# Optimization experiments

Measured on AMD Instinct MI355X. Metric: run time of the kernel, lower is better.

The kernel has to match this reference:

```python
import jax, jax.numpy as jnp
import numpy as np

N = 100_000      # nodes
D = 64           # in_dim
E = 1_600_000    # edges (avg degree 16)
P_L = 0.5        # leaky slope for low-pass gate
P_H = 0.5        # leaky slope for high-pass gate


def setup_inputs() -> dict:
    key = jax.random.key(0)
    ks = jax.random.split(key, 10)
    h = jax.random.normal(ks[0], (N, D), jnp.float32)
    d = jax.random.uniform(ks[1], (N,), jnp.float32)  # degree norms 1/sqrt(deg)
    src = jax.random.randint(ks[2], (E,), 0, N)
    dst = jax.random.randint(ks[3], (E,), 0, N)
    # xavier_normal(gain=1.414) scale ~ gain*sqrt(2/(fan_in+fan_out))
    sg = 1.414 * np.sqrt(2.0 / (2 * D + 1))
    sr = 1.414 * np.sqrt(2.0 / (2 * D + D))
    Wl = jax.random.normal(ks[4], (1, 2 * D), jnp.float32) * sg
    bl = jnp.zeros((1,), jnp.float32)
    Wh = jax.random.normal(ks[5], (1, 2 * D), jnp.float32) * sg
    bh = jnp.zeros((1,), jnp.float32)
    Wr = jax.random.normal(ks[6], (D, 2 * D), jnp.float32) * sr
    br = jnp.zeros((D,), jnp.float32)
    return {"h": h, "d": d, "src": src, "dst": dst,
            "Wl": Wl, "bl": bl, "Wh": Wh, "bh": bh, "Wr": Wr, "br": br}


def reference(h, d, src, dst, Wl, bl, Wh, bh, Wr, br):
    # gate_x(cat([h_dst, h_src])) == h_dst @ W[:, :D] + h_src @ W[:, D:] + b
    # -> project once per node [N], gather per edge [E] (avoids [E,2D] concat)
    low_dst = h @ Wl[0, :D]
    low_src = h @ Wl[0, D:]
    _low = low_dst[dst] + low_src[src] + bl[0]                     # [E]
    g_low = jnp.tanh(jax.nn.relu(jnp.where(_low > 0, _low, -P_L * _low)))

    high_dst = h @ Wh[0, :D]
    high_src = h @ Wh[0, D:]
    _high = high_dst[dst] + high_src[src] + bh[0]                  # [E]
    g_high = jnp.tanh(-jax.nn.relu(jnp.where(_high > 0, _high, -P_H * _high)))

    dd = d[dst] * d[src]                                           # [E]
    e_low = g_low * dd
    e_high = g_high * dd

    h_src = h[src]                                                 # [E, D]
    z_low = jax.ops.segment_sum(h_src * e_low[:, None], dst, num_segments=N)
    z_high = jax.ops.segment_sum(h_src * e_high[:, None], dst, num_segments=N)

    z = jnp.concatenate([z_low, z_high], axis=1)                   # [N, 2D]
    return z @ Wr.T + br                                           # [N, D]
```

## Files before the change

### kernel.cpp

```cpp
#include <hip/hip_runtime.h>
#include <hip/hip_fp16.h>
#include <math.h>

#define N_NODES 100000
#define D_DIM   64
#define N_EDGES 1600000
#define P_L 0.5f
#define P_H 0.5f

#define NPB   32
#define NB    3125
#define TILE  8192
#define NT    ((N_EDGES + TILE - 1) / TILE)
#define CAP   768
#define ZS    132

typedef unsigned int uint;
typedef unsigned short ushort_t;

__device__ inline ushort_t f2bf(float f) {
    uint u = __float_as_uint(f);
    uint r = (u + 0x7fffu + ((u >> 16) & 1u)) >> 16;
    return (ushort_t)r;
}

__device__ inline float tanh_pos(float x) {
    return 1.f - 2.f / (__expf(2.f * x) + 1.f);
}

__global__ __launch_bounds__(256) void node_gates_kernel(
    const float* __restrict__ h, const float* __restrict__ dvec,
    const float* __restrict__ Wl, const float* __restrict__ Wh,
    ushort_t* __restrict__ hbf,
    float4* __restrict__ gdst4, float4* __restrict__ gsrc4)
{
    int tid = threadIdx.x;
    int node = blockIdx.x * 4 + (tid >> 6);
    if (node >= N_NODES) return;
    int lane = tid & 63;

    float hv = h[(size_t)node * 64 + lane];
    hbf[(size_t)node * 64 + lane] = f2bf(hv);

    float pld = hv * Wl[lane];
    float pls = hv * Wl[64 + lane];
    float phd = hv * Wh[lane];
    float phs = hv * Wh[64 + lane];
    #pragma unroll
    for (int m = 32; m >= 1; m >>= 1) {
        pld += __shfl_xor(pld, m);
        pls += __shfl_xor(pls, m);
        phd += __shfl_xor(phd, m);
        phs += __shfl_xor(phs, m);
    }
    if (lane == 0) {
        float d = dvec[node];
        gdst4[node] = make_float4(pld, phd, d, 0.f);
        gsrc4[node] = make_float4(pls, phs, d, 0.f);
    }
}

__global__ __launch_bounds__(1024) void bucket_hist_kernel(const int* __restrict__ dst,
                                                           int* __restrict__ T) {
    __shared__ int hist[NB];
    int tid = threadIdx.x;
    for (int i = tid; i < NB; i += 1024) hist[i] = 0;
    __syncthreads();
    int base = blockIdx.x * TILE;
    #pragma unroll
    for (int j = 0; j < TILE / 1024; ++j) {
        int e = base + j * 1024 + tid;
        if (e < N_EDGES) atomicAdd(&hist[dst[e] >> 5], 1);
    }
    __syncthreads();
    int* row = T + (size_t)blockIdx.x * NB;
    for (int i = tid; i < NB; i += 1024) row[i] = hist[i];
}

__global__ __launch_bounds__(1024) void scanA_kernel(int* __restrict__ T,
                                                     int* __restrict__ totG) {
    int b = blockIdx.x * 1024 + threadIdx.x;
    if (b >= NB) return;
    int run = 0;
    for (int w = 0; w < NT; ++w) {
        int idx = w * NB + b;
        int v = T[idx];
        T[idx] = run;
        run += v;
    }
    totG[b] = run;
}

__global__ __launch_bounds__(1024) void scanB_kernel(const int* __restrict__ totG,
                                                     int* __restrict__ baseG,
                                                     int* __restrict__ bucketoffs,
                                                     const float* __restrict__ Wr,
                                                     float* __restrict__ wrt) {
    int tid = threadIdx.x;
    for (int idx = tid; idx < 64 * 128; idx += 1024) {
        int c = idx >> 7;
        int k = idx & 127;
        wrt[k * 64 + c] = Wr[idx];
    }

    __shared__ int scan_lds[1024];
    int a[4];
    int s = 0;
    #pragma unroll
    for (int i = 0; i < 4; ++i) {
        int b = tid * 4 + i;
        a[i] = (b < NB) ? totG[b] : 0;
        s += a[i];
    }
    scan_lds[tid] = s;
    __syncthreads();
    for (int d = 1; d < 1024; d <<= 1) {
        int v = (tid >= d) ? scan_lds[tid - d] : 0;
        __syncthreads();
        scan_lds[tid] += v;
        __syncthreads();
    }
    int excl = scan_lds[tid] - s;
    int total = scan_lds[1023];
    #pragma unroll
    for (int i = 0; i < 4; ++i) {
        int b = tid * 4 + i;
        if (b < NB) { baseG[b] = excl; bucketoffs[b] = excl; }
        excl += a[i];
    }
    if (tid == 0) bucketoffs[NB] = total;
}

__global__ __launch_bounds__(1024) void place_kernel(
    const int* __restrict__ src, const int* __restrict__ dst,
    const int* __restrict__ T, const int* __restrict__ baseG,
    const float4* __restrict__ gdst4, const float4* __restrict__ gsrc4,
    const float* __restrict__ bl, const float* __restrict__ bh,
    uint2* __restrict__ ebuf)
{
    __shared__ int cur[NB];
    int tid = threadIdx.x;
    const int* row = T + (size_t)blockIdx.x * NB;
    for (int i = tid; i < NB; i += 1024) cur[i] = row[i] + baseG[i];
    __syncthreads();

    float bl0 = bl[0], bh0 = bh[0];
    int base = blockIdx.x * TILE;
    #pragma unroll
    for (int j = 0; j < TILE / 1024; ++j) {
        int e = base + j * 1024 + tid;
        if (e >= N_EDGES) continue;
        int t = dst[e];
        int s = src[e];
        float4 gt = gdst4[t];
        float4 gs = gsrc4[s];
        float xl = gt.x + gs.x + bl0;
        float xh = gt.y + gs.y + bh0;
        float ll = xl > 0.f ? xl : -P_L * xl;
        float hh = xh > 0.f ? xh : -P_H * xh;
        float dd = gt.z * gs.z;
        float el =  tanh_pos(ll) * dd;
        float eh = -tanh_pos(hh) * dd;
        uint ge = (uint)__half_as_ushort(__float2half_rn(el))
                | ((uint)__half_as_ushort(__float2half_rn(eh)) << 16);
        int b  = t >> 5;
        uint dl = (uint)(t & 31);
        int pos = atomicAdd(&cur[b], 1);
        ebuf[pos] = make_uint2((uint)s | (dl << 17), ge);
    }
}

__global__ __launch_bounds__(512) void accum_final_kernel(
    const int* __restrict__ bucketoffs, const uint2* __restrict__ ebuf,
    const ushort_t* __restrict__ hbf, const float* __restrict__ wrt,
    const float* __restrict__ br, float* __restrict__ out)
{
    __shared__ float z[NPB * ZS];
    __shared__ uint2 srec[CAP];
    __shared__ int ncount[NPB];
    __shared__ int nbase[NPB];
    __shared__ int ncur[NPB];

    int tid = threadIdx.x;
    int bk = blockIdx.x;
    int beg = bucketoffs[bk];
    int end = bucketoffs[bk + 1];
    int cnt = end - beg;
    if (cnt > CAP) cnt = CAP;

    if (tid < NPB) ncount[tid] = 0;

    bool hA = tid < cnt;
    bool hB = tid + 512 < cnt;
    uint2 rA = hA ? ebuf[beg + tid] : make_uint2(0, 0);
    uint2 rB = hB ? ebuf[beg + tid + 512] : make_uint2(0, 0);
    __syncthreads();

    if (hA) atomicAdd(&ncount[(rA.x >> 17) & 31], 1);
    if (hB) atomicAdd(&ncount[(rB.x >> 17) & 31], 1);
    __syncthreads();

    if (tid < 32) {
        int v = ncount[tid];
        int p = v;
        #pragma unroll
        for (int d = 1; d < 32; d <<= 1) {
            int x = __shfl_up(p, d);
            if (tid >= d) p += x;
        }
        nbase[tid] = p - v;
        ncur[tid]  = p - v;
    }
    __syncthreads();

    if (hA) {
        int dl = (rA.x >> 17) & 31;
        srec[atomicAdd(&ncur[dl], 1)] = rA;
    }
    if (hB) {
        int dl = (rB.x >> 17) & 31;
        srec[atomicAdd(&ncur[dl], 1)] = rB;
    }
    __syncthreads();

    int sg = tid >> 3;
    int l8 = tid & 7;
    int node4 = sg >> 1;
    int par = sg & 1;
    int rbeg = nbase[node4];
    int rend = ncur[node4];

    float acc[16];
    #pragma unroll
    for (int j = 0; j < 16; ++j) acc[j] = 0.f;

    int k = rbeg + par;
    for (; k + 6 < rend; k += 8) {
        uint2 r0 = srec[k];
        uint2 r1 = srec[k + 2];
        uint2 r2 = srec[k + 4];
        uint2 r3 = srec[k + 6];
        uint4 h0 = *(const uint4*)(hbf + (size_t)(r0.x & 0x1FFFF) * 64 + l8 * 8);
        uint4 h1 = *(const uint4*)(hbf + (size_t)(r1.x & 0x1FFFF) * 64 + l8 * 8);
        uint4 h2 = *(const uint4*)(hbf + (size_t)(r2.x & 0x1FFFF) * 64 + l8 * 8);
        uint4 h3 = *(const uint4*)(hbf + (size_t)(r3.x & 0x1FFFF) * 64 + l8 * 8);

        #pragma unroll
        for (int u = 0; u < 4; ++u) {
            uint gy = (u == 0) ? r0.y : (u == 1) ? r1.y : (u == 2) ? r2.y : r3.y;
            uint4 hv = (u == 0) ? h0 : (u == 1) ? h1 : (u == 2) ? h2 : h3;
            float el = __half2float(__ushort_as_half((unsigned short)(gy & 0xffffu)));
            float eh = __half2float(__ushort_as_half((unsigned short)(gy >> 16)));
            float f0 = __uint_as_float(hv.x << 16);
            float f1 = __uint_as_float(hv.x & 0xffff0000u);
            float f2 = __uint_as_float(hv.y << 16);
            float f3 = __uint_as_float(hv.y & 0xffff0000u);
            float f4 = __uint_as_float(hv.z << 16);
            float f5 = __uint_as_float(hv.z & 0xffff0000u);
            float f6 = __uint_as_float(hv.w << 16);
            float f7 = __uint_as_float(hv.w & 0xffff0000u);
            acc[0]  += el * f0; acc[1]  += el * f1; acc[2]  += el * f2; acc[3]  += el * f3;
            acc[4]  += el * f4; acc[5]  += el * f5; acc[6]  += el * f6; acc[7]  += el * f7;
            acc[8]  += eh * f0; acc[9]  += eh * f1; acc[10] += eh * f2; acc[11] += eh * f3;
            acc[12] += eh * f4; acc[13] += eh * f5; acc[14] += eh * f6; acc[15] += eh * f7;
        }
    }
    for (; k < rend; k += 2) {
        uint2 r0 = srec[k];
        uint4 hv = *(const uint4*)(hbf + (size_t)(r0.x & 0x1FFFF) * 64 + l8 * 8);
        float el = __half2float(__ushort_as_half((unsigned short)(r0.y & 0xffffu)));
        float eh = __half2float(__ushort_as_half((unsigned short)(r0.y >> 16)));
        float f0 = __uint_as_float(hv.x << 16);
        float f1 = __uint_as_float(hv.x & 0xffff0000u);
        float f2 = __uint_as_float(hv.y << 16);
        float f3 = __uint_as_float(hv.y & 0xffff0000u);
        float f4 = __uint_as_float(hv.z << 16);
        float f5 = __uint_as_float(hv.z & 0xffff0000u);
        float f6 = __uint_as_float(hv.w << 16);
        float f7 = __uint_as_float(hv.w & 0xffff0000u);
        acc[0]  += el * f0; acc[1]  += el * f1; acc[2]  += el * f2; acc[3]  += el * f3;
        acc[4]  += el * f4; acc[5]  += el * f5; acc[6]  += el * f6; acc[7]  += el * f7;
        acc[8]  += eh * f0; acc[9]  += eh * f1; acc[10] += eh * f2; acc[11] += eh * f3;
        acc[12] += eh * f4; acc[13] += eh * f5; acc[14] += eh * f6; acc[15] += eh * f7;
    }

    float* zp = &z[node4 * ZS + l8 * 8];
    if (par == 0) {
        *(float4*)(zp + 0)  = make_float4(acc[0],  acc[1],  acc[2],  acc[3]);
        *(float4*)(zp + 4)  = make_float4(acc[4],  acc[5],  acc[6],  acc[7]);
        *(float4*)(zp + 64) = make_float4(acc[8],  acc[9],  acc[10], acc[11]);
        *(float4*)(zp + 68) = make_float4(acc[12], acc[13], acc[14], acc[15]);
    }
    __syncthreads();
    if (par == 1) {
        float4 z0 = *(float4*)(zp + 0);
        float4 z1 = *(float4*)(zp + 4);
        float4 z2 = *(float4*)(zp + 64);
        float4 z3 = *(float4*)(zp + 68);
        *(float4*)(zp + 0)  = make_float4(z0.x + acc[0],  z0.y + acc[1],  z0.z + acc[2],  z0.w + acc[3]);
        *(float4*)(zp + 4)  = make_float4(z1.x + acc[4],  z1.y + acc[5],  z1.z + acc[6],  z1.w + acc[7]);
        *(float4*)(zp + 64) = make_float4(z2.x + acc[8],  z2.y + acc[9],  z2.z + acc[10], z2.w + acc[11]);
        *(float4*)(zp + 68) = make_float4(z3.x + acc[12], z3.y + acc[13], z3.z + acc[14], z3.w + acc[15]);
    }
    __syncthreads();

    int node = tid >> 4;
    int g = tid & 15;
    float facc[4] = {0.f, 0.f, 0.f, 0.f};
    const float* zrow = z + node * ZS;
    #pragma unroll 4
    for (int kk = 0; kk < 128; ++kk) {
        float zv = zrow[kk];
        float4 w = *(const float4*)(wrt + kk * 64 + g * 4);
        facc[0] += zv * w.x; facc[1] += zv * w.y; facc[2] += zv * w.z; facc[3] += zv * w.w;
    }
    int n = bk * NPB + node;
    float* op = out + (size_t)n * 64 + g * 4;
    const float* bp = br + g * 4;
    *(float4*)(op) = make_float4(facc[0] + bp[0], facc[1] + bp[1], facc[2] + bp[2], facc[3] + bp[3]);
}

extern "C" void kernel_launch(void* const* d_in, const int* in_sizes, int n_in,
                              void* d_out, int out_size, void* d_ws, size_t ws_size,
                              hipStream_t stream) {
    const float* h    = (const float*)d_in[0];
    const float* dvec = (const float*)d_in[1];
    const int*   src  = (const int*)  d_in[2];
    const int*   dst  = (const int*)  d_in[3];
    const float* Wl   = (const float*)d_in[4];
    const float* bl   = (const float*)d_in[5];
    const float* Wh   = (const float*)d_in[6];
    const float* bh   = (const float*)d_in[7];
    const float* Wr   = (const float*)d_in[8];
    const float* br   = (const float*)d_in[9];
    float* out = (float*)d_out;

    char* ws = (char*)d_ws;
    size_t off = 0;
    auto alloc = [&](size_t bytes) { char* p = ws + off; off += (bytes + 255) & ~size_t(255); return p; };

    ushort_t* hbf       = (ushort_t*)alloc((size_t)N_NODES * 64 * 2);
    float4*   gdst4     = (float4*)  alloc((size_t)N_NODES * 16);
    float4*   gsrc4     = (float4*)  alloc((size_t)N_NODES * 16);
    float*    wrt       = (float*)   alloc(64 * 128 * 4);
    int*      T         = (int*)     alloc((size_t)NT * NB * 4);
    int*      totG      = (int*)     alloc((size_t)NB * 4);
    int*      baseG     = (int*)     alloc((size_t)NB * 4);
    int*      bucketoffs= (int*)     alloc((size_t)(NB + 1) * 4);
    uint2*    ebuf      = (uint2*)   alloc((size_t)N_EDGES * 8);

    node_gates_kernel<<<(N_NODES + 3) / 4, 256, 0, stream>>>(h, dvec, Wl, Wh, hbf, gdst4, gsrc4);
    bucket_hist_kernel<<<NT, 1024, 0, stream>>>(dst, T);
    scanA_kernel<<<(NB + 1023) / 1024, 1024, 0, stream>>>(T, totG);
    scanB_kernel<<<1, 1024, 0, stream>>>(totG, baseG, bucketoffs, Wr, wrt);
    place_kernel<<<NT, 1024, 0, stream>>>(src, dst, T, baseG, gdst4, gsrc4, bl, bh, ebuf);
    accum_final_kernel<<<NB, 512, 0, stream>>>(bucketoffs, ebuf, hbf, wrt, br, out);
}
```

Before: 317.2 us.

## Split column scan into two-level grouped scan and deepen gather unroll

The serial per-bucket scan over all 196 histogram tiles becomes a two-level scan: 28 groups of 7 tiles are scanned in parallel, then a second pass scans the group totals. The place kernel adds the group offset back when it initializes its cursors. In the accumulate kernel, the gather loop now issues 8 independent row loads per step instead of 4, and a launch-bounds occupancy hint is added. This targets the latency of the nearly serial scan (only 4 blocks, 196 dependent iterations) and raises memory-level parallelism in the gather, at the cost of one extra kernel launch and possibly more register pressure.

```diff
diff --git a/kernel.cpp b/kernel.cpp
--- a/kernel.cpp
+++ b/kernel.cpp
@@ -12,8 +12,11 @@
 #define NB    3125
 #define TILE  8192
 #define NT    ((N_EDGES + TILE - 1) / TILE)
+#define GRP   28
+#define GT    7
 #define CAP   768
 #define ZS    132
+
 
 typedef unsigned int uint;
 typedef unsigned short ushort_t;
@@ -26,6 +29,23 @@
 
 __device__ inline float tanh_pos(float x) {
     return 1.f - 2.f / (__expf(2.f * x) + 1.f);
+}
+
+__device__ inline void fma16(uint gy, uint4 hv, float* acc) {
+    float el = __half2float(__ushort_as_half((unsigned short)(gy & 0xffffu)));
+    float eh = __half2float(__ushort_as_half((unsigned short)(gy >> 16)));
+    float f0 = __uint_as_float(hv.x << 16);
+    float f1 = __uint_as_float(hv.x & 0xffff0000u);
+    float f2 = __uint_as_float(hv.y << 16);
+    float f3 = __uint_as_float(hv.y & 0xffff0000u);
+    float f4 = __uint_as_float(hv.z << 16);
+    float f5 = __uint_as_float(hv.z & 0xffff0000u);
+    float f6 = __uint_as_float(hv.w << 16);
+    float f7 = __uint_as_float(hv.w & 0xffff0000u);
+    acc[0]  += el * f0; acc[1]  += el * f1; acc[2]  += el * f2; acc[3]  += el * f3;
+    acc[4]  += el * f4; acc[5]  += el * f5; acc[6]  += el * f6; acc[7]  += el * f7;
+    acc[8]  += eh * f0; acc[9]  += eh * f1; acc[10] += eh * f2; acc[11] += eh * f3;
+    acc[12] += eh * f4; acc[13] += eh * f5; acc[14] += eh * f6; acc[15] += eh * f7;
 }
 
 __global__ __launch_bounds__(256) void node_gates_kernel(
@@ -77,15 +97,32 @@
     for (int i = tid; i < NB; i += 1024) row[i] = hist[i];
 }
 
-__global__ __launch_bounds__(1024) void scanA_kernel(int* __restrict__ T,
-                                                     int* __restrict__ totG) {
+__global__ __launch_bounds__(1024) void scanA1_kernel(int* __restrict__ T,
+                                                      int* __restrict__ S) {
+    int b = blockIdx.x * 1024 + threadIdx.x;
+    if (b >= NB) return;
+    int g = blockIdx.y;
+    int run = 0;
+    #pragma unroll
+    for (int w = g * GT; w < g * GT + GT; ++w) {
+        int idx = w * NB + b;
+        int v = T[idx];
+        T[idx] = run;
+        run += v;
+    }
+    S[(size_t)g * NB + b] = run;
+}
+
+__global__ __launch_bounds__(1024) void scanA2_kernel(int* __restrict__ S,
+                                                      int* __restrict__ totG) {
     int b = blockIdx.x * 1024 + threadIdx.x;
     if (b >= NB) return;
     int run = 0;
-    for (int w = 0; w < NT; ++w) {
-        int idx = w * NB + b;
-        int v = T[idx];
-        T[idx] = run;
+    #pragma unroll
+    for (int g = 0; g < GRP; ++g) {
+        int idx = g * NB + b;
+        int v = S[idx];
+        S[idx] = run;
         run += v;
     }
     totG[b] = run;
@@ -133,15 +170,17 @@
 
 __global__ __launch_bounds__(1024) void place_kernel(
     const int* __restrict__ src, const int* __restrict__ dst,
-    const int* __restrict__ T, const int* __restrict__ baseG,
+    const int* __restrict__ T, const int* __restrict__ S,
+    const int* __restrict__ baseG,
     const float4* __restrict__ gdst4, const float4* __restrict__ gsrc4,
     const float* __restrict__ bl, const float* __restrict__ bh,
     uint2* __restrict__ ebuf)
 {
     __shared__ int cur[NB];
     int tid = threadIdx.x;
-    const int* row = T + (size_t)blockIdx.x * NB;
-    for (int i = tid; i < NB; i += 1024) cur[i] = row[i] + baseG[i];
+    const int* row  = T + (size_t)blockIdx.x * NB;
+    const int* Srow = S + (size_t)(blockIdx.x / GT) * NB;
+    for (int i = tid; i < NB; i += 1024) cur[i] = row[i] + Srow[i] + baseG[i];
     __syncthreads();
 
     float bl0 = bl[0], bh0 = bh[0];
@@ -170,7 +209,7 @@
     }
 }
 
-__global__ __launch_bounds__(512) void accum_final_kernel(
+__global__ __launch_bounds__(512, 8) void accum_final_kernel(
     const int* __restrict__ bucketoffs, const uint2* __restrict__ ebuf,
     const ushort_t* __restrict__ hbf, const float* __restrict__ wrt,
     const float* __restrict__ br, float* __restrict__ out)
@@ -235,53 +274,34 @@
     for (int j = 0; j < 16; ++j) acc[j] = 0.f;
 
     int k = rbeg + par;
-    for (; k + 6 < rend; k += 8) {
-        uint2 r0 = srec[k];
-        uint2 r1 = srec[k + 2];
-        uint2 r2 = srec[k + 4];
-        uint2 r3 = srec[k + 6];
-        uint4 h0 = *(const uint4*)(hbf + (size_t)(r0.x & 0x1FFFF) * 64 + l8 * 8);
-        uint4 h1 = *(const uint4*)(hbf + (size_t)(r1.x & 0x1FFFF) * 64 + l8 * 8);
-        uint4 h2 = *(const uint4*)(hbf + (size_t)(r2.x & 0x1FFFF) * 64 + l8 * 8);
-        uint4 h3 = *(const uint4*)(hbf + (size_t)(r3.x & 0x1FFFF) * 64 + l8 * 8);
-
-        #pragma unroll
-        for (int u = 0; u < 4; ++u) {
-            uint gy = (u == 0) ? r0.y : (u == 1) ? r1.y : (u == 2) ? r2.y : r3.y;
-            uint4 hv = (u == 0) ? h0 : (u == 1) ? h1 : (u == 2) ? h2 : h3;
-            float el = __half2float(__ushort_as_half((unsigned short)(gy & 0xffffu)));
-            float eh = __half2float(__ushort_as_half((unsigned short)(gy >> 16)));
-            float f0 = __uint_as_float(hv.x << 16);
-            float f1 = __uint_as_float(hv.x & 0xffff0000u);
-            float f2 = __uint_as_float(hv.y << 16);
-            float f3 = __uint_as_float(hv.y & 0xffff0000u);
-            float f4 = __uint_as_float(hv.z << 16);
-            float f5 = __uint_as_float(hv.z & 0xffff0000u);
-            float f6 = __uint_as_float(hv.w << 16);
-            float f7 = __uint_as_float(hv.w & 0xffff0000u);
-            acc[0]  += el * f0; acc[1]  += el * f1; acc[2]  += el * f2; acc[3]  += el * f3;
-            acc[4]  += el * f4; acc[5]  += el * f5; acc[6]  += el * f6; acc[7]  += el * f7;
-            acc[8]  += eh * f0; acc[9]  += eh * f1; acc[10] += eh * f2; acc[11] += eh * f3;
-            acc[12] += eh * f4; acc[13] += eh * f5; acc[14] += eh * f6; acc[15] += eh * f7;
+    while (k + 14 < rend) {
+        uint gy[8]; uint4 hh[8];
+        #pragma unroll
+        for (int i = 0; i < 8; ++i) {
+            uint2 r = srec[k + 2 * i];
+            gy[i] = r.y;
+            hh[i] = *(const uint4*)(hbf + (size_t)(r.x & 0x1FFFF) * 64 + l8 * 8);
         }
+        #pragma unroll
+        for (int i = 0; i < 8; ++i) fma16(gy[i], hh[i], acc);
+        k += 16;
+    }
+    while (k + 6 < rend) {
+        uint gy[4]; uint4 hh[4];
+        #pragma unroll
+        for (int i = 0; i < 4; ++i) {
+            uint2 r = srec[k + 2 * i];
+            gy[i] = r.y;
+            hh[i] = *(const uint4*)(hbf + (size_t)(r.x & 0x1FFFF) * 64 + l8 * 8);
+        }
+        #pragma unroll
+        for (int i = 0; i < 4; ++i) fma16(gy[i], hh[i], acc);
+        k += 8;
     }
     for (; k < rend; k += 2) {
         uint2 r0 = srec[k];
         uint4 hv = *(const uint4*)(hbf + (size_t)(r0.x & 0x1FFFF) * 64 + l8 * 8);
-        float el = __half2float(__ushort_as_half((unsigned short)(r0.y & 0xffffu)));
-        float eh = __half2float(__ushort_as_half((unsigned short)(r0.y >> 16)));
-        float f0 = __uint_as_float(hv.x << 16);
-        float f1 = __uint_as_float(hv.x & 0xffff0000u);
-        float f2 = __uint_as_float(hv.y << 16);
-        float f3 = __uint_as_float(hv.y & 0xffff0000u);
-        float f4 = __uint_as_float(hv.z << 16);
-        float f5 = __uint_as_float(hv.z & 0xffff0000u);
-        float f6 = __uint_as_float(hv.w << 16);
-        float f7 = __uint_as_float(hv.w & 0xffff0000u);
-        acc[0]  += el * f0; acc[1]  += el * f1; acc[2]  += el * f2; acc[3]  += el * f3;
-        acc[4]  += el * f4; acc[5]  += el * f5; acc[6]  += el * f6; acc[7]  += el * f7;
-        acc[8]  += eh * f0; acc[9]  += eh * f1; acc[10] += eh * f2; acc[11] += eh * f3;
-        acc[12] += eh * f4; acc[13] += eh * f5; acc[14] += eh * f6; acc[15] += eh * f7;
+        fma16(r0.y, hv, acc);
     }
 
     float* zp = &z[node4 * ZS + l8 * 8];
@@ -344,6 +364,7 @@
     float4*   gsrc4     = (float4*)  alloc((size_t)N_NODES * 16);
     float*    wrt       = (float*)   alloc(64 * 128 * 4);
     int*      T         = (int*)     alloc((size_t)NT * NB * 4);
+    int*      S         = (int*)     alloc((size_t)GRP * NB * 4);
     int*      totG      = (int*)     alloc((size_t)NB * 4);
     int*      baseG     = (int*)     alloc((size_t)NB * 4);
     int*      bucketoffs= (int*)     alloc((size_t)(NB + 1) * 4);
@@ -351,8 +372,12 @@
 
     node_gates_kernel<<<(N_NODES + 3) / 4, 256, 0, stream>>>(h, dvec, Wl, Wh, hbf, gdst4, gsrc4);
     bucket_hist_kernel<<<NT, 1024, 0, stream>>>(dst, T);
-    scanA_kernel<<<(NB + 1023) / 1024, 1024, 0, stream>>>(T, totG);
+    {
+        dim3 g1((NB + 1023) / 1024, GRP);
+        scanA1_kernel<<<g1, 1024, 0, stream>>>(T, S);
+    }
+    scanA2_kernel<<<(NB + 1023) / 1024, 1024, 0, stream>>>(S, totG);
     scanB_kernel<<<1, 1024, 0, stream>>>(totG, baseG, bucketoffs, Wr, wrt);
-    place_kernel<<<NT, 1024, 0, stream>>>(src, dst, T, baseG, gdst4, gsrc4, bl, bh, ebuf);
+    place_kernel<<<NT, 1024, 0, stream>>>(src, dst, T, S, baseG, gdst4, gsrc4, bl, bh, ebuf);
     accum_final_kernel<<<NB, 512, 0, stream>>>(bucketoffs, ebuf, hbf, wrt, br, out);
 }
```

After: 649.4 us. 2.05x slower.
